# Optimization experiments

Hardware: AMD Instinct MI355X
Metric: run time of the kernel (lower is better)

Reference implementation:

```python
import jax, jax.numpy as jnp
import numpy as np

EPS = 1e-5

def _pw1d(W, b, x):  # W (O,C), x (B,C,N) -> (B,O,N); 1x1 Conv1d
    return jnp.einsum('oc,bcn->bon', W, x) + b[None, :, None]

def _pw2d(W, b, x):  # W (O,C), x (B,C,N,K) -> (B,O,N,K); 1x1 Conv2d
    return jnp.einsum('oc,bcnk->bonk', W, x) + b[None, :, None, None]

def _bn(x, g, b, m, v):  # BatchNorm2d, eval mode, over channel axis 1
    scale = g / jnp.sqrt(v + EPS)
    return (x - m[None, :, None, None]) * scale[None, :, None, None] + b[None, :, None, None]

def _knn(pos, k):  # pos (B,3,N) -> idx (B,N,K) of nearest neighbors (incl. self)
    p = jnp.transpose(pos, (0, 2, 1))             # (B,N,3)
    sq = jnp.sum(p * p, axis=-1)                  # (B,N)
    d = sq[:, :, None] - 2.0 * jnp.einsum('bid,bjd->bij', p, p) + sq[:, None, :]
    _, idx = jax.lax.top_k(-d, k)
    return idx

def _gather(feat, idx):  # feat (B,C,N), idx (B,N,K) -> (B,C,N,K)
    return jax.vmap(lambda f, i: f[:, i])(feat, idx)


def setup_inputs() -> dict:
    key = jax.random.key(0)
    B, C, N, H, AH, K = 4, 64, 4096, 64, 256, 16
    ks = jax.random.split(key, 32)
    s = lambda i, shp, sc=0.05: jax.random.normal(ks[i], shp, dtype=jnp.float32) * sc
    u = lambda i, shp: jax.random.uniform(ks[i], shp, dtype=jnp.float32, minval=0.5, maxval=1.5)
    return {
        'x': jax.random.normal(ks[0], (B, 3, N), dtype=jnp.float32),
        'y': jax.random.normal(ks[1], (B, C, N), dtype=jnp.float32),
        'W_start': s(2, (C, C)), 'b_start': s(3, (C,)),
        'W_key': s(4, (C, C)), 'b_key': s(5, (C,)),
        'W_query': s(6, (C, 3)), 'b_query': s(7, (C,)),
        'P1': s(8, (H, 3)), 'pb1': s(9, (H,)),
        'bn1_g': u(10, (H,)), 'bn1_b': s(11, (H,)), 'bn1_m': s(12, (H,)), 'bn1_v': u(13, (H,)),
        'P2': s(14, (C, H)), 'pb2': s(15, (C,)),
        'A1': s(16, (AH, C)), 'ab1': s(17, (AH,)),
        'bn2_g': u(18, (AH,)), 'bn2_b': s(19, (AH,)), 'bn2_m': s(20, (AH,)), 'bn2_v': u(21, (AH,)),
        'A2': s(22, (C, AH)), 'ab2': s(23, (C,)),
        'W_end': s(24, (C, C)), 'b_end': s(25, (C,)),
        'n_knn': 16,
    }


def reference(x, y, W_start, b_start, W_key, b_key, W_query, b_query,
              P1, pb1, bn1_g, bn1_b, bn1_m, bn1_v, P2, pb2,
              A1, ab1, bn2_g, bn2_b, bn2_m, bn2_v, A2, ab2,
              W_end, b_end, n_knn):
    identity = y
    y1 = _pw1d(W_start, b_start, y)                 # linear_start, (B,C,N)
    idx = _knn(x, n_knn)                            # (B,N,K)
    key = _pw1d(W_key, b_key, y1)
    value = y1
    query = _pw1d(W_query, b_query, x)              # 3 -> C pointwise
    key_g = _gather(key, idx)                       # (B,C,N,K)
    qk_rel = query[..., None] - key_g
    pos_rel = x[..., None] - _gather(x, idx)        # (B,3,N,K)
    pe = _pw2d(P2, pb2, jax.nn.relu(_bn(_pw2d(P1, pb1, pos_rel), bn1_g, bn1_b, bn1_m, bn1_v)))
    attn = _pw2d(A2, ab2, jax.nn.relu(_bn(_pw2d(A1, ab1, qk_rel + pe), bn2_g, bn2_b, bn2_m, bn2_v)))
    attn = jax.nn.softmax(attn, axis=-1)            # softmax over neighbor axis
    val = value[..., None] + pe                     # (B,C,N,K)
    agg = jnp.sum(attn * val, axis=-1)              # einsum 'bcij,bcij->bci'
    out = _pw1d(W_end, b_end, agg) + identity
    return out
```

## Files before the change

kernel.cpp:

```cpp
#include <hip/hip_runtime.h>
#include <hip/hip_bf16.h>

#define BB 4
#define CC 64
#define NN 4096
#define HH 64
#define AH 256
#define KNN 16
#define EPSV 1e-5f

#define KNN_BLKS 2048
#define PF_BLKS 256
#define PP_BLKS 32

typedef __attribute__((ext_vector_type(8))) short short8;
typedef __attribute__((ext_vector_type(4))) short short4v;
typedef __attribute__((ext_vector_type(4))) unsigned short ushort4v;
typedef __attribute__((ext_vector_type(4))) float floatx4;

__device__ __forceinline__ unsigned short f2bf(float f) {
    unsigned u = __float_as_uint(f);
    u += 0x7FFFu + ((u >> 16) & 1u);
    return (unsigned short)(u >> 16);
}
__device__ __forceinline__ float bf2f(unsigned short u) {
    return __uint_as_float(((unsigned)u) << 16);
}
__device__ __forceinline__ unsigned long long umin64(unsigned long long a, unsigned long long b) {
    return a < b ? a : b;
}
__device__ __forceinline__ unsigned long long umax64(unsigned long long a, unsigned long long b) {
    return a > b ? a : b;
}
__device__ __forceinline__ unsigned long long shfl_xor_u64(unsigned long long v, int m) {
    int lo = __shfl_xor((int)(unsigned)(v & 0xFFFFFFFFull), m);
    int hi = __shfl_xor((int)(unsigned)(v >> 32), m);
    return ((unsigned long long)(unsigned)hi << 32) | (unsigned)lo;
}
__device__ __forceinline__ unsigned fmono(float d) {
    unsigned u = __float_as_uint(d);
    return ((int)u < 0) ? ~u : (u | 0x80000000u);
}

#define UPITCH 68
#define HPITCH 68

__device__ __forceinline__ short8 lds_frag(const unsigned short* p) {
    short4v lo = *(const short4v*)p;
    short4v hi = *(const short4v*)(p + 4);
    short8 v;
    v[0] = lo[0]; v[1] = lo[1]; v[2] = lo[2]; v[3] = lo[3];
    v[4] = hi[0]; v[5] = hi[1]; v[6] = hi[2]; v[7] = hi[3];
    return v;
}

__global__ __launch_bounds__(256) void fused_prep_knn(
    const float* __restrict__ x, const float* __restrict__ y,
    const float* __restrict__ Ws, const float* __restrict__ bs,
    const float* __restrict__ Wk, const float* __restrict__ bk,
    const float* __restrict__ Wq, const float* __restrict__ bq,
    const float* __restrict__ P1, const float* __restrict__ pb1,
    const float* __restrict__ P2, const float* __restrict__ A1,
    const float* __restrict__ ab1, const float* __restrict__ A2,
    const float* __restrict__ g1, const float* __restrict__ b1v,
    const float* __restrict__ m1, const float* __restrict__ v1,
    const float* __restrict__ g2, const float* __restrict__ b2v,
    const float* __restrict__ m2, const float* __restrict__ v2,
    const float* __restrict__ Wend,
    int* __restrict__ idx_out,
    unsigned short* __restrict__ y1bf, unsigned short* __restrict__ keybf,
    unsigned short* __restrict__ qrybf,
    unsigned short* __restrict__ A1L, unsigned short* __restrict__ A2L,
    unsigned short* __restrict__ P2L, unsigned short* __restrict__ WendL,
    float* __restrict__ P1p, float* __restrict__ ab1f, float* __restrict__ bn2s_c) {
    __shared__ __align__(16) char smem[65536];
    int blk = blockIdx.x;
    int lane = threadIdx.x & 63;
    int w = threadIdx.x >> 6;

    if (blk < KNN_BLKS) {
        float4* pts = (float4*)smem;
        unsigned long long* surv = (unsigned long long*)smem;

        int b = blk >> 9;
        int grp = blk & 511;
        const float* xb = x + (size_t)b * 3 * NN;
        for (int i = threadIdx.x; i < NN; i += 256) {
            float cx = xb[i], cy = xb[NN + i], cz = xb[2 * NN + i];
            pts[i] = make_float4(cx, cy, cz, cx * cx + cy * cy + cz * cz);
        }
        __syncthreads();

        int n0 = (grp << 3) + (w << 1);
        float4 q0 = pts[n0], q1 = pts[n0 + 1];
        float q0x = -2.f * q0.x, q0y = -2.f * q0.y, q0z = -2.f * q0.z, q0w = q0.w;
        float q1x = -2.f * q1.x, q1y = -2.f * q1.y, q1z = -2.f * q1.z, q1w = q1.w;

        float d0reg[64], d1reg[64];
        float vmin0 = 3.4e38f, vmin1 = 3.4e38f;
#pragma unroll
        for (int r = 0; r < 64; ++r) {
            float4 c = pts[(r << 6) + lane];
            float d0 = fmaf(q0x, c.x, fmaf(q0y, c.y, fmaf(q0z, c.z, c.w + q0w)));
            float d1 = fmaf(q1x, c.x, fmaf(q1y, c.y, fmaf(q1z, c.z, c.w + q1w)));
            d0reg[r] = d0; d1reg[r] = d1;
            vmin0 = fminf(vmin0, d0);
            vmin1 = fminf(vmin1, d1);
        }

        float T[2];
#pragma unroll
        for (int t = 0; t < 2; ++t) {
            float v = t ? vmin1 : vmin0;
#pragma unroll
            for (int k = 2; k <= 64; k <<= 1) {
#pragma unroll
                for (int j = k >> 1; j > 0; j >>= 1) {
                    float o = __shfl_xor(v, j);
                    bool lower = (lane & j) == 0;
                    bool up = (lane & k) == 0;
                    float mn = fminf(v, o), mx = fmaxf(v, o);
                    v = (lower == up) ? mn : mx;
                }
            }
            T[t] = __shfl(v, 15);
        }
        __syncthreads();

#pragma unroll
        for (int t = 0; t < 2; ++t) {
            float Tt = T[t];
            unsigned long long* buf = surv + (((w << 1) + t) << 7);
            unsigned cnt = 0;
#pragma unroll
            for (int r = 0; r < 64; ++r) {
                float d = t ? d1reg[r] : d0reg[r];
                bool hit = d <= Tt;
                unsigned long long mask = __ballot(hit);
                if (hit) {
                    unsigned off = cnt + (unsigned)__popcll(mask & ((1ull << lane) - 1ull));
                    if (off < 128) {
                        int j = (r << 6) + lane;
                        buf[off] = ((unsigned long long)fmono(d) << 32) | (unsigned)j;
                    }
                }
                cnt += (unsigned)__popcll(mask);
            }
            if (cnt > 128) cnt = 128;

            unsigned long long v0 = (lane < (int)cnt) ? buf[lane] : 0xFFFFFFFFFFFFFFFFull;
            unsigned long long v1 = (lane + 64 < (int)cnt) ? buf[lane + 64] : 0xFFFFFFFFFFFFFFFFull;
#pragma unroll
            for (int k = 2; k <= 128; k <<= 1) {
#pragma unroll
                for (int j = k >> 1; j > 0; j >>= 1) {
                    if (j >= 64) {
                        unsigned long long lo = umin64(v0, v1), hi = umax64(v0, v1);
                        v0 = lo; v1 = hi;
                    } else {
                        bool lower = (lane & j) == 0;
                        unsigned long long o0 = shfl_xor_u64(v0, j);
                        bool up0 = ((lane & k) == 0);
                        v0 = (lower == up0) ? umin64(v0, o0) : umax64(v0, o0);
                        unsigned long long o1 = shfl_xor_u64(v1, j);
                        bool up1 = (((64 + lane) & k) == 0);
                        v1 = (lower == up1) ? umin64(v1, o1) : umax64(v1, o1);
                    }
                }
            }
            if (lane < KNN)
                idx_out[((size_t)b * NN + n0 + t) * KNN + lane] =
                    (int)(unsigned)(v0 & 0xFFFFFFFFull);
        }
    } else if (blk < KNN_BLKS + PF_BLKS) {
        unsigned short* tl = (unsigned short*)smem + w * 16 * UPITCH;
        int g4 = (blk - KNN_BLKS) * 4 + w;
        int b = g4 >> 8;
        int n0 = (g4 & 255) << 4;
        int m = lane & 15, quad = lane >> 4;
        size_t ybase = (size_t)b * CC * NN;

        short8 yA[2];
#pragma unroll
        for (int ks = 0; ks < 2; ++ks)
#pragma unroll
            for (int j = 0; j < 8; ++j)
                yA[ks][j] = (short)f2bf(y[ybase + (size_t)(ks * 32 + quad * 8 + j) * NN + n0 + m]);

#pragma unroll
        for (int ot = 0; ot < 4; ++ot) {
            short8 bb0, bb1;
#pragma unroll
            for (int ks = 0; ks < 2; ++ks) {
                const float* wr = Ws + (ot * 16 + m) * CC + ks * 32 + quad * 8;
                float4 lo = *(const float4*)wr;
                float4 hi = *(const float4*)(wr + 4);
                short8 bb;
                bb[0] = (short)f2bf(lo.x); bb[1] = (short)f2bf(lo.y);
                bb[2] = (short)f2bf(lo.z); bb[3] = (short)f2bf(lo.w);
                bb[4] = (short)f2bf(hi.x); bb[5] = (short)f2bf(hi.y);
                bb[6] = (short)f2bf(hi.z); bb[7] = (short)f2bf(hi.w);
                if (ks == 0) bb0 = bb; else bb1 = bb;
            }
            floatx4 acc = (floatx4){0.f, 0.f, 0.f, 0.f};
            acc = __builtin_amdgcn_mfma_f32_16x16x32_bf16(yA[0], bb0, acc, 0, 0, 0);
            acc = __builtin_amdgcn_mfma_f32_16x16x32_bf16(yA[1], bb1, acc, 0, 0, 0);
            float bsv = bs[ot * 16 + m];
#pragma unroll
            for (int r = 0; r < 4; ++r)
                tl[(4 * quad + r) * UPITCH + ot * 16 + m] = f2bf(acc[r] + bsv);
        }
        __syncthreads();

        short8 uA[2];
#pragma unroll
        for (int ks = 0; ks < 2; ++ks)
            uA[ks] = lds_frag(&tl[m * UPITCH + ks * 32 + quad * 8]);

        int p = lane >> 2, ck = lane & 3;
        size_t obase = ((size_t)b * NN + n0 + p) * CC + ck * 16;
#pragma unroll
        for (int s = 0; s < 4; ++s)
            *(ushort4v*)(y1bf + obase + s * 4) =
                *(const ushort4v*)&tl[p * UPITCH + ck * 16 + s * 4];
        __syncthreads();

#pragma unroll
        for (int ot = 0; ot < 4; ++ot) {
            short8 bb0, bb1;
#pragma unroll
            for (int ks = 0; ks < 2; ++ks) {
                const float* wr = Wk + (ot * 16 + m) * CC + ks * 32 + quad * 8;
                float4 lo = *(const float4*)wr;
                float4 hi = *(const float4*)(wr + 4);
                short8 bb;
                bb[0] = (short)f2bf(lo.x); bb[1] = (short)f2bf(lo.y);
                bb[2] = (short)f2bf(lo.z); bb[3] = (short)f2bf(lo.w);
                bb[4] = (short)f2bf(hi.x); bb[5] = (short)f2bf(hi.y);
                bb[6] = (short)f2bf(hi.z); bb[7] = (short)f2bf(hi.w);
                if (ks == 0) bb0 = bb; else bb1 = bb;
            }
            floatx4 acc = (floatx4){0.f, 0.f, 0.f, 0.f};
            acc = __builtin_amdgcn_mfma_f32_16x16x32_bf16(uA[0], bb0, acc, 0, 0, 0);
            acc = __builtin_amdgcn_mfma_f32_16x16x32_bf16(uA[1], bb1, acc, 0, 0, 0);
            float bkv = bk[ot * 16 + m];
#pragma unroll
            for (int r = 0; r < 4; ++r)
                tl[(4 * quad + r) * UPITCH + ot * 16 + m] = f2bf(acc[r] + bkv);
        }
        __syncthreads();
#pragma unroll
        for (int s = 0; s < 4; ++s)
            *(ushort4v*)(keybf + obase + s * 4) =
                *(const ushort4v*)&tl[p * UPITCH + ck * 16 + s * 4];

        float x0 = x[(size_t)(b * 3 + 0) * NN + n0 + p];
        float x1 = x[(size_t)(b * 3 + 1) * NN + n0 + p];
        float x2 = x[(size_t)(b * 3 + 2) * NN + n0 + p];
#pragma unroll
        for (int s = 0; s < 4; ++s) {
            ushort4v pk;
#pragma unroll
            for (int e = 0; e < 4; ++e) {
                int ch = ck * 16 + s * 4 + e;
                pk[e] = f2bf(Wq[3 * ch + 0] * x0 + Wq[3 * ch + 1] * x1 +
                             Wq[3 * ch + 2] * x2 + bq[ch]);
            }
            *(ushort4v*)(qrybf + obase + s * 4) = pk;
        }
    } else {
        int pb = blk - KNN_BLKS - PF_BLKS;
        int t0 = threadIdx.x;
        int t = pb * 256 + t0;
        const int stride = PP_BLKS * 256;
        if (pb == 0) {
            if (t0 < HH) {
                float s = g1[t0] * rsqrtf(v1[t0] + EPSV);
                float c = b1v[t0] - m1[t0] * s;
                P1p[4 * t0 + 0] = P1[3 * t0 + 0] * s;
                P1p[4 * t0 + 1] = P1[3 * t0 + 1] * s;
                P1p[4 * t0 + 2] = P1[3 * t0 + 2] * s;
                P1p[4 * t0 + 3] = pb1[t0] * s + c;
            }
            if (t0 < AH) {
                float s = g2[t0] * rsqrtf(v2[t0] + EPSV);
                bn2s_c[t0] = s;
                ab1f[t0] = ab1[t0] * s + (b2v[t0] - m2[t0] * s);
            }
        }
        for (int i = t; i < 16384; i += stride) {
            int e = i & 7, ln = (i >> 3) & 63, ks = (i >> 9) & 1, ht = i >> 10;
            int m = ln & 15, q = ln >> 4;
            A1L[i] = f2bf(A1[(ht * 16 + m) * CC + ks * 32 + q * 8 + e]);
        }
        for (int i = t; i < 16384; i += stride) {
            int e = i & 7, ln = (i >> 3) & 63, kk = (i >> 9) & 7, nt = i >> 12;
            int m = ln & 15, q = ln >> 4;
            A2L[i] = f2bf(A2[(nt * 16 + m) * AH + kk * 32 + q * 8 + e]);
        }
        for (int i = t; i < 4096; i += stride) {
            int e = i & 7, ln = (i >> 3) & 63, ks = (i >> 9) & 1, nt = i >> 10;
            int m = ln & 15, q = ln >> 4;
            P2L[i] = f2bf(P2[(nt * 16 + m) * HH + ks * 32 + q * 8 + e]);
        }
        for (int i = t; i < 4096; i += stride) {
            int e = i & 7, ln = (i >> 3) & 63, ks = (i >> 9) & 1, wv = i >> 10;
            int m = ln & 15, q = ln >> 4;
            WendL[i] = f2bf(Wend[(wv * 16 + m) * CC + ks * 32 + q * 8 + e]);
        }
    }
}

__global__ __launch_bounds__(256, 3) void attn_mfma(
    const float* __restrict__ x, const float* __restrict__ y,
    const unsigned short* __restrict__ y1bf, const unsigned short* __restrict__ keybf,
    const unsigned short* __restrict__ qrybf, const int* __restrict__ idx,
    const float* __restrict__ P1p, const unsigned short* __restrict__ P2L,
    const float* __restrict__ pb2, const unsigned short* __restrict__ A1L,
    const float* __restrict__ ab1f, const float* __restrict__ bn2s_c,
    const unsigned short* __restrict__ A2L, const unsigned short* __restrict__ WendL,
    const float* __restrict__ bend,
    float* __restrict__ out) {
    __shared__ unsigned short u_lds[128 * UPITCH];
    __shared__ unsigned short hid_lds[128 * HPITCH];
    __shared__ float agg_lds[8 * 68];
    __shared__ float outstage[512];

    int blk = blockIdx.x;
    int b = blk & 3;
    int n0 = (blk >> 2) << 3;
    int w = threadIdx.x >> 6;
    int lane = threadIdx.x & 63;
    int m = lane & 15, quad = lane >> 4;

    int pt[2];
    size_t bpt[2];
#pragma unroll
    for (int t = 0; t < 2; ++t) {
        pt[t] = n0 + 2 * w + t;
        bpt[t] = (size_t)b * NN + pt[t];
    }

    int jm[2], j4[2][4];
    unsigned short qu[2][4], kvu[2][4][4];
#pragma unroll
    for (int t = 0; t < 2; ++t) {
        jm[t] = idx[bpt[t] * KNN + m];
#pragma unroll
        for (int r = 0; r < 4; ++r) j4[t][r] = idx[bpt[t] * KNN + 4 * quad + r];
#pragma unroll
        for (int nt = 0; nt < 4; ++nt) {
            qu[t][nt] = qrybf[bpt[t] * CC + nt * 16 + m];
#pragma unroll
            for (int r = 0; r < 4; ++r)
                kvu[t][nt][r] = keybf[((size_t)b * NN + j4[t][r]) * CC + nt * 16 + m];
        }
    }

    short8 h1A[2][2];
#pragma unroll
    for (int t = 0; t < 2; ++t) {
        float dx = x[(size_t)(b * 3 + 0) * NN + pt[t]] - x[(size_t)(b * 3 + 0) * NN + jm[t]];
        float dy = x[(size_t)(b * 3 + 1) * NN + pt[t]] - x[(size_t)(b * 3 + 1) * NN + jm[t]];
        float dz = x[(size_t)(b * 3 + 2) * NN + pt[t]] - x[(size_t)(b * 3 + 2) * NN + jm[t]];
#pragma unroll
        for (int ks = 0; ks < 2; ++ks)
#pragma unroll
            for (int j = 0; j < 8; ++j) {
                int h1 = ks * 32 + quad * 8 + j;
                const float4 p = *(const float4*)(P1p + 4 * h1);
                float a = fmaxf(p.x * dx + p.y * dy + p.z * dz + p.w, 0.f);
                h1A[t][ks][j] = (short)f2bf(a);
            }
    }

    floatx4 pacc[2][4];
#pragma unroll
    for (int t = 0; t < 2; ++t)
#pragma unroll
        for (int nt = 0; nt < 4; ++nt) pacc[t][nt] = (floatx4){0.f, 0.f, 0.f, 0.f};
#pragma unroll
    for (int ks = 0; ks < 2; ++ks)
#pragma unroll
        for (int nt = 0; nt < 4; ++nt) {
            short8 bb = *(const short8*)(P2L + ((nt * 2 + ks) * 64 + lane) * 8);
            pacc[0][nt] = __builtin_amdgcn_mfma_f32_16x16x32_bf16(h1A[0][ks], bb, pacc[0][nt], 0, 0, 0);
            pacc[1][nt] = __builtin_amdgcn_mfma_f32_16x16x32_bf16(h1A[1][ks], bb, pacc[1][nt], 0, 0, 0);
        }
#pragma unroll
    for (int nt = 0; nt < 4; ++nt) {
        float pb = pb2[nt * 16 + m];
#pragma unroll
        for (int t = 0; t < 2; ++t)
#pragma unroll
            for (int r = 0; r < 4; ++r) pacc[t][nt][r] += pb;
    }

#pragma unroll
    for (int t = 0; t < 2; ++t)
#pragma unroll
        for (int nt = 0; nt < 4; ++nt) {
            float qv = bf2f(qu[t][nt]);
#pragma unroll
            for (int r = 0; r < 4; ++r) {
                float uu = qv - bf2f(kvu[t][nt][r]) + pacc[t][nt][r];
                u_lds[(w * 32 + t * 16 + 4 * quad + r) * UPITCH + nt * 16 + m] = f2bf(uu);
            }
        }

    short8 uA[2][2];
#pragma unroll
    for (int t = 0; t < 2; ++t)
#pragma unroll
        for (int ks = 0; ks < 2; ++ks)
            uA[t][ks] = lds_frag(&u_lds[(w * 32 + t * 16 + m) * UPITCH + ks * 32 + quad * 8]);

    floatx4 acc2[2][4];
#pragma unroll
    for (int t = 0; t < 2; ++t)
#pragma unroll
        for (int nt = 0; nt < 4; ++nt) acc2[t][nt] = (floatx4){0.f, 0.f, 0.f, 0.f};

    for (int qd = 0; qd < 4; ++qd) {
#pragma unroll
        for (int nt4 = 0; nt4 < 4; ++nt4) {
            int ht = qd * 4 + nt4;
            const unsigned short* a1t = A1L + ht * 1024 + lane * 8;
            short8 b0 = *(const short8*)(a1t);
            short8 b1 = *(const short8*)(a1t + 512);
            int h = ht * 16 + m;
            float s = bn2s_c[h], t0 = ab1f[h];
#pragma unroll
            for (int t = 0; t < 2; ++t) {
                floatx4 acc = (floatx4){0.f, 0.f, 0.f, 0.f};
                acc = __builtin_amdgcn_mfma_f32_16x16x32_bf16(uA[t][0], b0, acc, 0, 0, 0);
                acc = __builtin_amdgcn_mfma_f32_16x16x32_bf16(uA[t][1], b1, acc, 0, 0, 0);
#pragma unroll
                for (int r = 0; r < 4; ++r) {
                    float hv = fmaxf(acc[r] * s + t0, 0.f);
                    hid_lds[(w * 32 + t * 16 + 4 * quad + r) * HPITCH + nt4 * 16 + m] = f2bf(hv);
                }
            }
        }
        short8 hA[2][2];
#pragma unroll
        for (int t = 0; t < 2; ++t)
#pragma unroll
            for (int ks = 0; ks < 2; ++ks)
                hA[t][ks] = lds_frag(&hid_lds[(w * 32 + t * 16 + m) * HPITCH + ks * 32 + quad * 8]);
#pragma unroll
        for (int ks = 0; ks < 2; ++ks)
#pragma unroll
            for (int nt = 0; nt < 4; ++nt) {
                int kk = qd * 2 + ks;
                short8 bb = *(const short8*)(A2L + ((nt * 8 + kk) * 64 + lane) * 8);
                acc2[0][nt] = __builtin_amdgcn_mfma_f32_16x16x32_bf16(hA[0][ks], bb, acc2[0][nt], 0, 0, 0);
                acc2[1][nt] = __builtin_amdgcn_mfma_f32_16x16x32_bf16(hA[1][ks], bb, acc2[1][nt], 0, 0, 0);
            }
    }

#pragma unroll
    for (int t = 0; t < 2; ++t)
#pragma unroll
        for (int nt = 0; nt < 4; ++nt) {
            float l0 = acc2[t][nt][0], l1 = acc2[t][nt][1];
            float l2 = acc2[t][nt][2], l3 = acc2[t][nt][3];
            float mx = fmaxf(fmaxf(l0, l1), fmaxf(l2, l3));
            mx = fmaxf(mx, __shfl_xor(mx, 16));
            mx = fmaxf(mx, __shfl_xor(mx, 32));
            float e0 = __expf(l0 - mx), e1 = __expf(l1 - mx);
            float e2 = __expf(l2 - mx), e3 = __expf(l3 - mx);
            float sum = (e0 + e1) + (e2 + e3);
            sum += __shfl_xor(sum, 16);
            sum += __shfl_xor(sum, 32);
            float y1v = bf2f(y1bf[bpt[t] * CC + nt * 16 + m]);
            float contrib = e0 * (y1v + pacc[t][nt][0]) + e1 * (y1v + pacc[t][nt][1]) +
                            e2 * (y1v + pacc[t][nt][2]) + e3 * (y1v + pacc[t][nt][3]);
            contrib += __shfl_xor(contrib, 16);
            contrib += __shfl_xor(contrib, 32);
            float agg = contrib / sum;
            if (quad == 0) agg_lds[(2 * w + t) * 68 + nt * 16 + m] = agg;
        }
    __syncthreads();

    short8 aggA[2];
#pragma unroll
    for (int ks = 0; ks < 2; ++ks)
#pragma unroll
        for (int j = 0; j < 8; ++j)
            aggA[ks][j] = (short)f2bf(agg_lds[(m & 7) * 68 + ks * 32 + quad * 8 + j]);
    short8 wb0 = *(const short8*)(WendL + ((w * 2 + 0) * 64 + lane) * 8);
    short8 wb1 = *(const short8*)(WendL + ((w * 2 + 1) * 64 + lane) * 8);
    floatx4 facc = (floatx4){0.f, 0.f, 0.f, 0.f};
    facc = __builtin_amdgcn_mfma_f32_16x16x32_bf16(aggA[0], wb0, facc, 0, 0, 0);
    facc = __builtin_amdgcn_mfma_f32_16x16x32_bf16(aggA[1], wb1, facc, 0, 0, 0);
    if (quad < 2) {
        float be = bend[w * 16 + m];
#pragma unroll
        for (int r = 0; r < 4; ++r)
            outstage[(w * 16 + m) * 8 + 4 * quad + r] = facc[r] + be;
    }
    __syncthreads();

    int t2 = threadIdx.x;
    int o = t2 >> 2, pp = (t2 & 3) * 2;
#pragma unroll
    for (int e = 0; e < 2; ++e) {
        size_t oi = ((size_t)(b * CC + o)) * NN + n0 + pp + e;
        out[oi] = outstage[o * 8 + pp + e] + y[oi];
    }
}

extern "C" void kernel_launch(void* const* d_in, const int* in_sizes, int n_in,
                              void* d_out, int out_size, void* d_ws, size_t ws_size,
                              hipStream_t stream) {
    const float* x    = (const float*)d_in[0];
    const float* y    = (const float*)d_in[1];
    const float* Ws   = (const float*)d_in[2];
    const float* bs   = (const float*)d_in[3];
    const float* Wk   = (const float*)d_in[4];
    const float* bk   = (const float*)d_in[5];
    const float* Wq   = (const float*)d_in[6];
    const float* bq   = (const float*)d_in[7];
    const float* P1   = (const float*)d_in[8];
    const float* pb1  = (const float*)d_in[9];
    const float* g1   = (const float*)d_in[10];
    const float* b1   = (const float*)d_in[11];
    const float* m1   = (const float*)d_in[12];
    const float* v1   = (const float*)d_in[13];
    const float* P2   = (const float*)d_in[14];
    const float* pb2  = (const float*)d_in[15];
    const float* A1   = (const float*)d_in[16];
    const float* ab1  = (const float*)d_in[17];
    const float* g2   = (const float*)d_in[18];
    const float* b2   = (const float*)d_in[19];
    const float* m2   = (const float*)d_in[20];
    const float* v2   = (const float*)d_in[21];
    const float* A2   = (const float*)d_in[22];
    const float* ab2  = (const float*)d_in[23];
    const float* Wend = (const float*)d_in[24];
    const float* bend = (const float*)d_in[25];
    (void)ab2;

    unsigned short* usws = (unsigned short*)d_ws;
    unsigned short* y1bf  = usws;
    unsigned short* keybf = usws + 1048576;
    unsigned short* qrybf = usws + 2097152;
    int* idx = (int*)(usws + 3145728);
    unsigned short* A1L = usws + 3670016;
    unsigned short* A2L = A1L + 16384;
    unsigned short* P2L = A2L + 16384;
    unsigned short* WendL = P2L + 4096;
    float* P1p   = (float*)(WendL + 4096);
    float* ab1f  = P1p + 256;
    float* bn2sc = ab1f + 256;
    float* out   = (float*)d_out;

    hipLaunchKernelGGL(fused_prep_knn, dim3(KNN_BLKS + PF_BLKS + PP_BLKS), dim3(256), 0, stream,
                       x, y, Ws, bs, Wk, bk, Wq, bq,
                       P1, pb1, P2, A1, ab1, A2,
                       g1, b1, m1, v1, g2, b2, m2, v2, Wend,
                       idx, y1bf, keybf, qrybf,
                       A1L, A2L, P2L, WendL, P1p, ab1f, bn2sc);
    hipLaunchKernelGGL(attn_mfma, dim3(2048), dim3(256), 0, stream,
                       x, y, y1bf, keybf, qrybf, idx,
                       P1p, P2L, pb2, A1L, ab1f, bn2sc, A2L, WendL,
                       bend, out);
}
```

Measured before the change: 216.7 us.

## Shrink kNN LDS footprint with SoA points and add fast 64-survivor sort path

```diff
diff --git a/kernel.cpp b/kernel.cpp
--- a/kernel.cpp
+++ b/kernel.cpp
@@ -54,7 +54,7 @@
     return v;
 }
 
-__global__ __launch_bounds__(256) void fused_prep_knn(
+__global__ __launch_bounds__(256, 3) void fused_prep_knn(
     const float* __restrict__ x, const float* __restrict__ y,
     const float* __restrict__ Ws, const float* __restrict__ bs,
     const float* __restrict__ Wk, const float* __restrict__ bk,
@@ -73,39 +73,57 @@
     unsigned short* __restrict__ A1L, unsigned short* __restrict__ A2L,
     unsigned short* __restrict__ P2L, unsigned short* __restrict__ WendL,
     float* __restrict__ P1p, float* __restrict__ ab1f, float* __restrict__ bn2s_c) {
-    __shared__ __align__(16) char smem[65536];
+    __shared__ __align__(16) char smem[49152];
     int blk = blockIdx.x;
     int lane = threadIdx.x & 63;
     int w = threadIdx.x >> 6;
 
     if (blk < KNN_BLKS) {
-        float4* pts = (float4*)smem;
+        float* px = (float*)smem;
+        float* py = px + NN;
+        float* pz = py + NN;
         unsigned long long* surv = (unsigned long long*)smem;
 
         int b = blk >> 9;
         int grp = blk & 511;
         const float* xb = x + (size_t)b * 3 * NN;
         for (int i = threadIdx.x; i < NN; i += 256) {
-            float cx = xb[i], cy = xb[NN + i], cz = xb[2 * NN + i];
-            pts[i] = make_float4(cx, cy, cz, cx * cx + cy * cy + cz * cz);
+            px[i] = xb[i];
+            py[i] = xb[NN + i];
+            pz[i] = xb[2 * NN + i];
         }
         __syncthreads();
 
         int n0 = (grp << 3) + (w << 1);
-        float4 q0 = pts[n0], q1 = pts[n0 + 1];
-        float q0x = -2.f * q0.x, q0y = -2.f * q0.y, q0z = -2.f * q0.z, q0w = q0.w;
-        float q1x = -2.f * q1.x, q1y = -2.f * q1.y, q1z = -2.f * q1.z, q1w = q1.w;
+        float q0x = px[n0], q0y = py[n0], q0z = pz[n0];
+        float q1x = px[n0 + 1], q1y = py[n0 + 1], q1z = pz[n0 + 1];
+        float q0w = q0x * q0x + q0y * q0y + q0z * q0z;
+        float q1w = q1x * q1x + q1y * q1y + q1z * q1z;
+        q0x *= -2.f; q0y *= -2.f; q0z *= -2.f;
+        q1x *= -2.f; q1y *= -2.f; q1z *= -2.f;
 
         float d0reg[64], d1reg[64];
         float vmin0 = 3.4e38f, vmin1 = 3.4e38f;
 #pragma unroll
-        for (int r = 0; r < 64; ++r) {
-            float4 c = pts[(r << 6) + lane];
-            float d0 = fmaf(q0x, c.x, fmaf(q0y, c.y, fmaf(q0z, c.z, c.w + q0w)));
-            float d1 = fmaf(q1x, c.x, fmaf(q1y, c.y, fmaf(q1z, c.z, c.w + q1w)));
-            d0reg[r] = d0; d1reg[r] = d1;
-            vmin0 = fminf(vmin0, d0);
-            vmin1 = fminf(vmin1, d1);
+        for (int r = 0; r < 16; ++r) {
+            int c = r * 64 + lane;
+            float4 cx = ((const float4*)px)[c];
+            float4 cy = ((const float4*)py)[c];
+            float4 cz = ((const float4*)pz)[c];
+            float exv[4] = {cx.x, cx.y, cx.z, cx.w};
+            float eyv[4] = {cy.x, cy.y, cy.z, cy.w};
+            float ezv[4] = {cz.x, cz.y, cz.z, cz.w};
+#pragma unroll
+            for (int e = 0; e < 4; ++e) {
+                float nx = exv[e], ny = eyv[e], nz = ezv[e];
+                float nc = nx * nx + ny * ny + nz * nz;
+                float d0 = fmaf(q0x, nx, fmaf(q0y, ny, fmaf(q0z, nz, nc + q0w)));
+                float d1 = fmaf(q1x, nx, fmaf(q1y, ny, fmaf(q1z, nz, nc + q1w)));
+                d0reg[r * 4 + e] = d0;
+                d1reg[r * 4 + e] = d1;
+                vmin0 = fminf(vmin0, d0);
+                vmin1 = fminf(vmin1, d1);
+            }
         }
 
         float T[2];
@@ -133,14 +151,14 @@
             unsigned long long* buf = surv + (((w << 1) + t) << 7);
             unsigned cnt = 0;
 #pragma unroll
-            for (int r = 0; r < 64; ++r) {
-                float d = t ? d1reg[r] : d0reg[r];
+            for (int s = 0; s < 64; ++s) {
+                float d = t ? d1reg[s] : d0reg[s];
                 bool hit = d <= Tt;
                 unsigned long long mask = __ballot(hit);
                 if (hit) {
                     unsigned off = cnt + (unsigned)__popcll(mask & ((1ull << lane) - 1ull));
                     if (off < 128) {
-                        int j = (r << 6) + lane;
+                        int j = ((s >> 2) * 64 + lane) * 4 + (s & 3);
                         buf[off] = ((unsigned long long)fmono(d) << 32) | (unsigned)j;
                     }
                 }
@@ -149,22 +167,36 @@
             if (cnt > 128) cnt = 128;
 
             unsigned long long v0 = (lane < (int)cnt) ? buf[lane] : 0xFFFFFFFFFFFFFFFFull;
-            unsigned long long v1 = (lane + 64 < (int)cnt) ? buf[lane + 64] : 0xFFFFFFFFFFFFFFFFull;
-#pragma unroll
-            for (int k = 2; k <= 128; k <<= 1) {
-#pragma unroll
-                for (int j = k >> 1; j > 0; j >>= 1) {
-                    if (j >= 64) {
-                        unsigned long long lo = umin64(v0, v1), hi = umax64(v0, v1);
-                        v0 = lo; v1 = hi;
-                    } else {
+            if (cnt <= 64) {
+#pragma unroll
+                for (int k = 2; k <= 64; k <<= 1) {
+#pragma unroll
+                    for (int j = k >> 1; j > 0; j >>= 1) {
                         bool lower = (lane & j) == 0;
+                        bool up = (lane & k) == 0;
                         unsigned long long o0 = shfl_xor_u64(v0, j);
-                        bool up0 = ((lane & k) == 0);
-                        v0 = (lower == up0) ? umin64(v0, o0) : umax64(v0, o0);
-                        unsigned long long o1 = shfl_xor_u64(v1, j);
-                        bool up1 = (((64 + lane) & k) == 0);
-                        v1 = (lower == up1) ? umin64(v1, o1) : umax64(v1, o1);
+                        v0 = (lower == up) ? umin64(v0, o0) : umax64(v0, o0);
+                    }
+                }
+            } else {
+                unsigned long long v1 = (lane + 64 < (int)cnt) ? buf[lane + 64]
+                                                               : 0xFFFFFFFFFFFFFFFFull;
+#pragma unroll
+                for (int k = 2; k <= 128; k <<= 1) {
+#pragma unroll
+                    for (int j = k >> 1; j > 0; j >>= 1) {
+                        if (j >= 64) {
+                            unsigned long long lo = umin64(v0, v1), hi = umax64(v0, v1);
+                            v0 = lo; v1 = hi;
+                        } else {
+                            bool lower = (lane & j) == 0;
+                            unsigned long long o0 = shfl_xor_u64(v0, j);
+                            bool up0 = ((lane & k) == 0);
+                            v0 = (lower == up0) ? umin64(v0, o0) : umax64(v0, o0);
+                            unsigned long long o1 = shfl_xor_u64(v1, j);
+                            bool up1 = (((64 + lane) & k) == 0);
+                            v1 = (lower == up1) ? umin64(v1, o1) : umax64(v1, o1);
+                        }
                     }
                 }
             }
```

Result: faster. 199.3 us (-8.0%).
